# Optimization experiments

Measured on AMD Instinct MI355X. Metric: run time of the kernel, lower is better.

## Reference

```python
import jax, jax.numpy as jnp
import numpy as np

INPUT_DIM, HIDDEN_DIM, N_CLASSES = 512, 256, 2
TOP_RATIO, MIN_PATCHES, K_INST = 0.7, 128, 8
B, N = 4, 16384


def setup_inputs() -> dict:
    key = jax.random.key(0)
    ks = jax.random.split(key, 10)
    D, H, C = INPUT_DIM, HIDDEN_DIM, N_CLASSES
    s = lambda fan: 1.0 / np.sqrt(fan)
    return {
        "features": jax.random.normal(ks[0], (B, N, D), dtype=jnp.float32),
        # attention_net: Linear(D->H) (dropout is identity in eval)
        "Wa": jax.random.uniform(ks[1], (D, H), minval=-s(D), maxval=s(D), dtype=jnp.float32),
        "ba": jax.random.uniform(ks[2], (H,), minval=-s(D), maxval=s(D), dtype=jnp.float32),
        # per-class attention branches: Linear(H->1), stacked over classes
        "Wbr": jax.random.uniform(ks[3], (C, H), minval=-s(H), maxval=s(H), dtype=jnp.float32),
        "bbr": jax.random.uniform(ks[4], (C,), minval=-s(H), maxval=s(H), dtype=jnp.float32),
        # per-class instance classifiers: Linear(D->H) -> ReLU -> Linear(H->2)
        "W1": jax.random.uniform(ks[5], (C, D, H), minval=-s(D), maxval=s(D), dtype=jnp.float32),
        "b1": jax.random.uniform(ks[6], (C, H), minval=-s(D), maxval=s(D), dtype=jnp.float32),
        "W2": jax.random.uniform(ks[7], (C, H, 2), minval=-s(H), maxval=s(H), dtype=jnp.float32),
        "b2": jax.random.uniform(ks[8], (C, 2), minval=-s(H), maxval=s(H), dtype=jnp.float32),
    }


def reference(features, Wa, ba, Wbr, bbr, W1, b1, W2, b2):
    Bb, Nn, D = features.shape
    C = Wbr.shape[0]

    # ---- compute_attention ----
    h = jax.nn.relu(features @ Wa + ba)                       # (B,N,H)
    a_logits = jnp.einsum('bnh,ch->bcn', h, Wbr) + bbr[None, :, None]
    attn_all = jax.nn.softmax(a_logits, axis=-1)              # (B,C,N)
    combined = attn_all.mean(axis=1)                          # (B,N)

    # ---- per-sample top-k selection (k static under jit) ----
    k = min(max(int(Nn * TOP_RATIO), MIN_PATCHES), Nn)
    _, sel_idx = jax.lax.top_k(combined, k)                   # (B,k)
    sel_idx = jnp.sort(sel_idx, axis=-1)
    selected = jnp.take_along_axis(features, sel_idx[..., None], axis=1)  # (B,k,D)

    # ---- instance clustering loss (vectorized over B x C) ----
    kk = min(K_INST, Nn // 2)
    _, top_idx = jax.lax.top_k(attn_all, kk)                  # (B,C,kk)
    _, bot_idx = jax.lax.top_k(-attn_all, kk)                 # largest=False
    both_idx = jnp.concatenate([top_idx, bot_idx], axis=-1)   # (B,C,2kk)
    inst = features[jnp.arange(Bb)[:, None, None], both_idx]  # (B,C,2kk,D)
    h1 = jax.nn.relu(jnp.einsum('bckd,cdh->bckh', inst, W1) + b1[None, :, None, :])
    logits = jnp.einsum('bckh,cho->bcko', h1, W2) + b2[None, :, None, :]  # (B,C,2kk,2)
    labels = jnp.concatenate([jnp.ones(kk, jnp.int32), jnp.zeros(kk, jnp.int32)])
    logp = jax.nn.log_softmax(logits, axis=-1)
    ce = -jnp.take_along_axis(
        logp, jnp.broadcast_to(labels[None, None, :, None], (Bb, C, 2 * kk, 1)), axis=-1
    )[..., 0]                                                 # (B,C,2kk)
    cl_loss = ce.mean(axis=-1).sum() / (Bb * C)

    return selected, combined, sel_idx, cl_loss
```

## Files before the change

### kernel.cpp

```cpp
#include <hip/hip_runtime.h>

#define NB 4
#define NP 16384
#define DD 512
#define HH 256
#define CC 2
#define KSEL 11468
#define TOTP (NB*NP)
#define BCAP 4096

#define OFF_COMB (NB*KSEL*DD)
#define OFF_IDX  (OFF_COMB + NB*NP)
#define OFF_LOSS (OFF_IDX + NB*KSEL)

#define WS_ALOGIT 0
#define WS_ATTN   (NB*CC*NP)
#define WS_SELIDX (2*NB*CC*NP)
#define WS_MZ     (WS_SELIDX + NB*KSEL)
#define WS_BCNT   (WS_MZ + 16)
#define WS_BLIST  (WS_BCNT + 4)
#define WS_TOP16  (WS_BLIST + NB*BCAP)
#define WS_CE     (WS_TOP16 + 128)

typedef __attribute__((ext_vector_type(8))) short short8x;
typedef __attribute__((ext_vector_type(4))) float f32x4;

__device__ __forceinline__ unsigned short f2bf(float x){
  unsigned u = __float_as_uint(x);
  unsigned r = (u + 0x7FFFu + ((u >> 16) & 1u)) >> 16;
  return (unsigned short)r;
}

__global__ __launch_bounds__(256) void waconv_kernel(
    const float* __restrict__ Wa, unsigned short* __restrict__ WaT)
{
  __shared__ float tile[32][33];
  const int tx = threadIdx.x, ty = threadIdx.y;
  const int k0 = blockIdx.x * 32, n0 = blockIdx.y * 32;
  #pragma unroll
  for (int i=0;i<4;++i)
    tile[ty+8*i][tx] = Wa[(size_t)(k0+ty+8*i)*HH + n0 + tx];
  __syncthreads();
  #pragma unroll
  for (int i=0;i<4;++i)
    WaT[(size_t)(n0+ty+8*i)*DD + k0 + tx] = f2bf(tile[tx][ty+8*i]);
}

__global__ __launch_bounds__(512) void gemm_mfma_kernel(
    const float* __restrict__ feat, const unsigned short* __restrict__ WaT,
    const float* __restrict__ ba, const float* __restrict__ Wbr,
    const float* __restrict__ bbr, float* __restrict__ aL)
{
  __shared__ __attribute__((aligned(16))) unsigned char smem[65536];
  __shared__ float sBA[HH], sW0[HH], sW1[HH];
  unsigned char* sA = smem;
  unsigned char* sB = smem + 16384;

  const int tid  = threadIdx.x;
  const int lane = tid & 63;
  const int wid  = tid >> 6;
  const int wm = wid >> 2, wn = wid & 3;
  const int fr = lane & 15, fq = lane >> 4;
  const int p0 = blockIdx.x * 128;
  const float bb0 = bbr[0], bb1 = bbr[1];

  if (tid < HH){ sBA[tid] = ba[tid]; sW0[tid] = Wbr[tid]; sW1[tid] = Wbr[HH+tid]; }

  f32x4 acc[4][4];
  #pragma unroll
  for (int i=0;i<4;++i)
    #pragma unroll
    for (int j=0;j<4;++j)
      acc[i][j] = (f32x4){0.f,0.f,0.f,0.f};

  const int am = tid >> 2, akq = (tid & 3) * 16;
  const int bn = tid >> 1, bhf = tid & 1;

  for (int k0 = 0; k0 < DD; k0 += 64){
    __syncthreads();
    {
      const float4* src = reinterpret_cast<const float4*>(
          feat + (size_t)(p0 + am)*DD + k0 + akq);
      float4 v0 = src[0], v1 = src[1], v2 = src[2], v3 = src[3];
      unsigned short u[16];
      u[0]=f2bf(v0.x); u[1]=f2bf(v0.y); u[2]=f2bf(v0.z); u[3]=f2bf(v0.w);
      u[4]=f2bf(v1.x); u[5]=f2bf(v1.y); u[6]=f2bf(v1.z); u[7]=f2bf(v1.w);
      u[8]=f2bf(v2.x); u[9]=f2bf(v2.y); u[10]=f2bf(v2.z); u[11]=f2bf(v2.w);
      u[12]=f2bf(v3.x); u[13]=f2bf(v3.y); u[14]=f2bf(v3.z); u[15]=f2bf(v3.w);
      uint4 w0, w1;
      w0.x = (unsigned)u[0] | ((unsigned)u[1]<<16);
      w0.y = (unsigned)u[2] | ((unsigned)u[3]<<16);
      w0.z = (unsigned)u[4] | ((unsigned)u[5]<<16);
      w0.w = (unsigned)u[6] | ((unsigned)u[7]<<16);
      w1.x = (unsigned)u[8] | ((unsigned)u[9]<<16);
      w1.y = (unsigned)u[10] | ((unsigned)u[11]<<16);
      w1.z = (unsigned)u[12] | ((unsigned)u[13]<<16);
      w1.w = (unsigned)u[14] | ((unsigned)u[15]<<16);
      const int swz = (am & 7) << 4;
      *reinterpret_cast<uint4*>(sA + (((am*128) + akq*2) ^ swz)) = w0;
      *reinterpret_cast<uint4*>(sA + (((am*128) + akq*2 + 16) ^ swz)) = w1;
    }
    {
      const uint4* src = reinterpret_cast<const uint4*>(
          WaT + (size_t)bn*DD + k0 + bhf*32);
      uint4 q0 = src[0], q1 = src[1], q2 = src[2], q3 = src[3];
      const int swz = (bn & 7) << 4;
      const int base = bn*128 + bhf*64;
      *reinterpret_cast<uint4*>(sB + ((base     ) ^ swz)) = q0;
      *reinterpret_cast<uint4*>(sB + ((base + 16) ^ swz)) = q1;
      *reinterpret_cast<uint4*>(sB + ((base + 32) ^ swz)) = q2;
      *reinterpret_cast<uint4*>(sB + ((base + 48) ^ swz)) = q3;
    }
    __syncthreads();
    #pragma unroll
    for (int kf = 0; kf < 2; ++kf){
      short8x af[4], bf[4];
      #pragma unroll
      for (int mf = 0; mf < 4; ++mf){
        int m_loc = wm*64 + mf*16 + fr;
        int off = ((m_loc*128 + kf*64 + fq*16) ^ ((m_loc & 7) << 4));
        af[mf] = *reinterpret_cast<const short8x*>(sA + off);
      }
      #pragma unroll
      for (int nf = 0; nf < 4; ++nf){
        int n_loc = wn*64 + nf*16 + fr;
        int off = ((n_loc*128 + kf*64 + fq*16) ^ ((n_loc & 7) << 4));
        bf[nf] = *reinterpret_cast<const short8x*>(sB + off);
      }
      #pragma unroll
      for (int mf = 0; mf < 4; ++mf)
        #pragma unroll
        for (int nf = 0; nf < 4; ++nf)
          acc[mf][nf] = __builtin_amdgcn_mfma_f32_16x16x32_bf16(
              af[mf], bf[nf], acc[mf][nf], 0, 0, 0);
    }
  }
  __syncthreads();

  float* hS = reinterpret_cast<float*>(smem);
  #pragma unroll
  for (int mh = 0; mh < 2; ++mh){
    if (wm == mh){
      #pragma unroll
      for (int mf = 0; mf < 4; ++mf)
        #pragma unroll
        for (int nf = 0; nf < 4; ++nf)
          #pragma unroll
          for (int r = 0; r < 4; ++r){
            int row = mf*16 + fq*4 + r;
            int col = wn*64 + nf*16 + fr;
            hS[row*256 + col] = acc[mf][nf][r];
          }
    }
    __syncthreads();
    {
      const int row = tid >> 3, cg = tid & 7;
      float s0 = 0.f, s1 = 0.f;
      #pragma unroll
      for (int j = 0; j < 8; ++j){
        int col = cg*4 + j*32;
        float4 hv = *reinterpret_cast<const float4*>(&hS[row*256 + col]);
        float xs[4] = {hv.x, hv.y, hv.z, hv.w};
        #pragma unroll
        for (int u = 0; u < 4; ++u){
          int ccol = col + u;
          float x = fmaxf(xs[u] + sBA[ccol], 0.f);
          s0 += x * sW0[ccol];
          s1 += x * sW1[ccol];
        }
      }
      s0 += __shfl_xor(s0,1); s1 += __shfl_xor(s1,1);
      s0 += __shfl_xor(s0,2); s1 += __shfl_xor(s1,2);
      s0 += __shfl_xor(s0,4); s1 += __shfl_xor(s1,4);
      if (cg == 0){
        int p = p0 + mh*64 + row;
        int b = p >> 14, nl = p & (NP-1);
        aL[((size_t)b*CC + 0)*NP + nl] = s0 + bb0;
        aL[((size_t)b*CC + 1)*NP + nl] = s1 + bb1;
      }
    }
    __syncthreads();
  }
}

__global__ __launch_bounds__(1024) void smstat_kernel(
    const float* __restrict__ aL, float* __restrict__ mz)
{
  __shared__ float  s_redf[16];
  __shared__ double s_redd[16];
  __shared__ float  s_max;
  const int tid = threadIdx.x;
  const int lane = tid & 63, wid = tid >> 6;
  const int r = blockIdx.x;
  const float* a = aL + (size_t)r*NP;
  float m = -1e30f;
  for (int n=tid; n<NP; n+=1024) m = fmaxf(m, a[n]);
  #pragma unroll
  for (int off=1; off<64; off<<=1) m = fmaxf(m, __shfl_xor(m, off));
  if (lane==0) s_redf[wid]=m;
  __syncthreads();
  if (tid==0){ float mm=s_redf[0]; for(int w=1;w<16;++w) mm=fmaxf(mm,s_redf[w]); s_max=mm; }
  __syncthreads();
  m = s_max;
  double ls = 0.0;
  for (int n=tid;n<NP;n+=1024) ls += (double)expf(a[n]-m);
  #pragma unroll
  for (int off=1; off<64; off<<=1) ls += __shfl_xor(ls, off);
  if (lane==0) s_redd[wid]=ls;
  __syncthreads();
  if (tid==0){
    double t=0; for(int w=0;w<16;++w) t+=s_redd[w];
    mz[r*2+0]=m; mz[r*2+1]=(float)(1.0/t);
  }
}

__global__ __launch_bounds__(1024) void selTF_kernel(
    const float* __restrict__ aL, const float* __restrict__ mz,
    float* __restrict__ attn, float* __restrict__ comb,
    int* __restrict__ bcnt, int* __restrict__ blist)
{
  __shared__ unsigned s_red[2][16];
  __shared__ int s_cnt;
  const int tid = threadIdx.x;
  const int b = blockIdx.x;
  const int lane = tid & 63, wid = tid >> 6;
  const float m0 = mz[b*4+0], iz0 = mz[b*4+1], m1 = mz[b*4+2], iz1 = mz[b*4+3];
  const float* a0 = aL + ((size_t)b*CC + 0)*NP;
  const float* a1 = aL + ((size_t)b*CC + 1)*NP;
  float* o0 = attn + ((size_t)b*CC + 0)*NP;
  float* o1 = attn + ((size_t)b*CC + 1)*NP;
  float* oc = comb + (size_t)b*NP;
  const int n0 = tid*16;

  unsigned v[16];
  #pragma unroll
  for (int g=0; g<4; ++g){
    float4 qa = *reinterpret_cast<const float4*>(a0 + n0 + g*4);
    float4 qb = *reinterpret_cast<const float4*>(a1 + n0 + g*4);
    float4 E0, E1, CV;
    E0.x = expf(qa.x-m0)*iz0; E1.x = expf(qb.x-m1)*iz1; CV.x = 0.5f*(E0.x+E1.x);
    E0.y = expf(qa.y-m0)*iz0; E1.y = expf(qb.y-m1)*iz1; CV.y = 0.5f*(E0.y+E1.y);
    E0.z = expf(qa.z-m0)*iz0; E1.z = expf(qb.z-m1)*iz1; CV.z = 0.5f*(E0.z+E1.z);
    E0.w = expf(qa.w-m0)*iz0; E1.w = expf(qb.w-m1)*iz1; CV.w = 0.5f*(E0.w+E1.w);
    *reinterpret_cast<float4*>(o0 + n0 + g*4) = E0;
    *reinterpret_cast<float4*>(o1 + n0 + g*4) = E1;
    *reinterpret_cast<float4*>(oc + n0 + g*4) = CV;
    v[g*4+0]=__float_as_uint(CV.x);
    v[g*4+1]=__float_as_uint(CV.y);
    v[g*4+2]=__float_as_uint(CV.z);
    v[g*4+3]=__float_as_uint(CV.w);
  }
  if (tid==0) s_cnt = 0;

  unsigned cur = 0;
  #pragma unroll 1
  for (int bit=31; bit>=12; --bit){
    unsigned trial = cur | (1u<<bit);
    int c = 0;
    #pragma unroll
    for (int i=0;i<16;++i) c += (v[i] >= trial) ? 1 : 0;
    #pragma unroll
    for (int off=1; off<64; off<<=1) c += __shfl_xor(c, off);
    if (lane==0) s_red[bit&1][wid] = (unsigned)c;
    __syncthreads();
    unsigned tot=0;
    #pragma unroll
    for (int w=0;w<16;++w) tot += s_red[bit&1][w];
    if (tot >= KSEL) cur = trial;
  }
  const float Tv = __uint_as_float(cur);
  const float lo = Tv*0.989f, hi = Tv*1.0115f;
  #pragma unroll
  for (int i=0;i<16;++i){
    float x = __uint_as_float(v[i]);
    if (x >= lo && x <= hi){
      int s = atomicAdd(&s_cnt, 1);
      if (s < BCAP) blist[b*BCAP + s] = n0 + i;
    }
  }
  __syncthreads();
  if (tid==0) bcnt[b] = (s_cnt < BCAP) ? s_cnt : BCAP;
}

__global__ __launch_bounds__(256) void recomp_kernel(
    const float* __restrict__ feat, const float* __restrict__ Wa,
    const float* __restrict__ ba, const float* __restrict__ Wbr,
    const float* __restrict__ bbr, const float* __restrict__ mz,
    const int* __restrict__ bcnt, const int* __restrict__ blist,
    float* __restrict__ comb)
{
  __shared__ float fS[DD];
  __shared__ float r0[4], r1[4];
  const int tid = threadIdx.x;
  const int b = blockIdx.x >> 12;
  const int s = blockIdx.x & (BCAP-1);
  if (s >= bcnt[b]) return;
  const int lane = tid & 63, wid = tid >> 6;
  const float m0 = mz[b*4+0], iz0 = mz[b*4+1], m1 = mz[b*4+2], iz1 = mz[b*4+3];
  const int n = blist[b*BCAP + s];
  if (tid < 128){
    float4 v = *reinterpret_cast<const float4*>(feat + ((size_t)b*NP + n)*DD + tid*4);
    *reinterpret_cast<float4*>(&fS[tid*4]) = v;
  }
  __syncthreads();
  float a0=0.f,a1=0.f,a2=0.f,a3=0.f;
  #pragma unroll 4
  for (int d=0; d<DD; d+=4){
    a0 += fS[d+0]*Wa[(size_t)(d+0)*HH + tid];
    a1 += fS[d+1]*Wa[(size_t)(d+1)*HH + tid];
    a2 += fS[d+2]*Wa[(size_t)(d+2)*HH + tid];
    a3 += fS[d+3]*Wa[(size_t)(d+3)*HH + tid];
  }
  float h = fmaxf((a0+a1)+(a2+a3) + ba[tid], 0.f);
  float p0 = h*Wbr[tid], p1 = h*Wbr[HH+tid];
  #pragma unroll
  for (int off=1; off<64; off<<=1){ p0+=__shfl_xor(p0,off); p1+=__shfl_xor(p1,off); }
  if (lane==0){ r0[wid]=p0; r1[wid]=p1; }
  __syncthreads();
  if (tid==0){
    float l0 = (r0[0]+r0[1])+(r0[2]+r0[3]) + bbr[0];
    float l1 = (r1[0]+r1[1])+(r1[2]+r1[3]) + bbr[1];
    comb[(size_t)b*NP + n] = 0.5f*(expf(l0-m0)*iz0 + expf(l1-m1)*iz1);
  }
}

__global__ __launch_bounds__(1024) void select_kernel(
    const float* __restrict__ comb, float* __restrict__ outIdxF,
    int* __restrict__ selIdx)
{
  __shared__ unsigned s_red[2][16];
  __shared__ unsigned s_wsum[16];
  const int tid = threadIdx.x;
  const int b = blockIdx.x;
  const int lane = tid & 63, wid = tid >> 6;
  const float* row = comb + (size_t)b*NP;

  unsigned v[16];
  {
    const float4* rp = reinterpret_cast<const float4*>(row + tid*16);
    #pragma unroll
    for (int g=0; g<4; ++g){
      float4 q = rp[g];
      v[g*4+0]=__float_as_uint(q.x);
      v[g*4+1]=__float_as_uint(q.y);
      v[g*4+2]=__float_as_uint(q.z);
      v[g*4+3]=__float_as_uint(q.w);
    }
  }
  unsigned cur = 0;
  #pragma unroll 1
  for (int bit=31; bit>=0; --bit){
    unsigned trial = cur | (1u<<bit);
    int c = 0;
    #pragma unroll
    for (int i=0;i<16;++i) c += (v[i] >= trial) ? 1 : 0;
    #pragma unroll
    for (int off=1; off<64; off<<=1) c += __shfl_xor(c, off);
    if (lane==0) s_red[bit&1][wid] = (unsigned)c;
    __syncthreads();
    unsigned tot=0;
    #pragma unroll
    for (int w=0;w<16;++w) tot += s_red[bit&1][w];
    if (tot >= KSEL) cur = trial;
  }
  const unsigned T = cur;
  {
    int c = 0;
    #pragma unroll
    for (int i=0;i<16;++i) c += (v[i] > T) ? 1 : 0;
    #pragma unroll
    for (int off=1; off<64; off<<=1) c += __shfl_xor(c, off);
    if (lane==0) s_red[1][wid] = (unsigned)c;
  }
  __syncthreads();
  unsigned gtot=0;
  #pragma unroll
  for (int w=0;w<16;++w) gtot += s_red[1][w];
  const int extra = KSEL - (int)gtot;

  int eqc=0;
  #pragma unroll
  for (int i=0;i<16;++i) eqc += (v[i]==T) ? 1 : 0;
  unsigned inc = (unsigned)eqc;
  #pragma unroll
  for (int off=1; off<64; off<<=1){
    unsigned o = __shfl_up(inc, off);
    if (lane >= off) inc += o;
  }
  if (lane==63) s_wsum[wid] = inc;
  __syncthreads();
  unsigned wbase = 0;
  for (int w=0; w<wid; ++w) wbase += s_wsum[w];
  const int eqBase = (int)(wbase + inc) - eqc;

  int eq=eqBase, sc=0;
  #pragma unroll
  for (int i=0;i<16;++i){
    unsigned x = v[i];
    if (x==T){ if (eq<extra) sc++; eq++; }
    else if (x>T) sc++;
  }
  unsigned inc2 = (unsigned)sc;
  #pragma unroll
  for (int off=1; off<64; off<<=1){
    unsigned o = __shfl_up(inc2, off);
    if (lane >= off) inc2 += o;
  }
  __syncthreads();
  if (lane==63) s_wsum[wid] = inc2;
  __syncthreads();
  unsigned wbase2 = 0;
  for (int w=0; w<wid; ++w) wbase2 += s_wsum[w];
  int pos = (int)(wbase2 + inc2) - sc;

  eq=eqBase;
  #pragma unroll
  for (int i=0;i<16;++i){
    unsigned x = v[i];
    int f=0;
    if (x==T){ if (eq<extra) f=1; eq++; }
    else if (x>T) f=1;
    if (f){
      int n = tid*16 + i;
      outIdxF[(size_t)b*KSEL + pos] = (float)n;
      selIdx[(size_t)b*KSEL + pos] = n;
      pos++;
    }
  }
}

__global__ __launch_bounds__(256) void gather_kernel(
    const float* __restrict__ feat, const int* __restrict__ selIdx,
    float* __restrict__ outSel)
{
  const int tid = threadIdx.x;
  const int row = blockIdx.x*2 + (tid>>7);
  const int c4 = tid & 127;
  const int b = row / KSEL;
  const int idx = selIdx[row];
  const float4 v = *reinterpret_cast<const float4*>(feat + ((size_t)b*NP + idx)*DD + c4*4);
  *reinterpret_cast<float4*>(outSel + (size_t)row*DD + c4*4) = v;
}

__global__ __launch_bounds__(256) void top16_kernel(
    const float* __restrict__ attn, int* __restrict__ top16)
{
  __shared__ unsigned long long wkT[4][8];
  __shared__ unsigned long long wkB[4][8];
  const int tid = threadIdx.x;
  const int bid = blockIdx.x;
  const int lane = tid & 63, wid = tid >> 6;
  const float* a = attn + (size_t)bid*NP;

  unsigned long long t8[8], b8[8];
  #pragma unroll
  for (int i=0;i<8;++i){ t8[i]=0ull; b8[i]=~0ull; }

  for (int j=0;j<16;++j){
    const int n4 = tid + 256*j;
    const float4 v = *reinterpret_cast<const float4*>(a + 4*n4);
    const float xs[4] = {v.x, v.y, v.z, v.w};
    #pragma unroll
    for (int q=0;q<4;++q){
      const int n = 4*n4 + q;
      const unsigned vb = __float_as_uint(xs[q]);
      unsigned long long kt = ((unsigned long long)vb<<32) | (unsigned)(NP-1-n);
      if (kt > t8[7]){
        t8[7]=kt;
        #pragma unroll
        for (int i=7;i>0;--i){ if (t8[i]>t8[i-1]){ unsigned long long t=t8[i-1]; t8[i-1]=t8[i]; t8[i]=t; } }
      }
      unsigned long long kb = ((unsigned long long)vb<<32) | (unsigned)n;
      if (kb < b8[7]){
        b8[7]=kb;
        #pragma unroll
        for (int i=7;i>0;--i){ if (b8[i]<b8[i-1]){ unsigned long long t=b8[i-1]; b8[i-1]=b8[i]; b8[i]=t; } }
      }
    }
  }

  #pragma unroll
  for (int pick=0; pick<8; ++pick){
    unsigned long long loc = t8[0];
    #pragma unroll
    for (int i=1;i<8;++i) loc = t8[i]>loc ? t8[i] : loc;
    #pragma unroll
    for (int off=1; off<64; off<<=1){ unsigned long long o=__shfl_xor(loc,off); loc=o>loc?o:loc; }
    if (lane==0) wkT[wid][pick]=loc;
    #pragma unroll
    for (int i=0;i<8;++i) if (t8[i]==loc) t8[i]=0ull;
  }
  #pragma unroll
  for (int pick=0; pick<8; ++pick){
    unsigned long long loc = b8[0];
    #pragma unroll
    for (int i=1;i<8;++i) loc = b8[i]<loc ? b8[i] : loc;
    #pragma unroll
    for (int off=1; off<64; off<<=1){ unsigned long long o=__shfl_xor(loc,off); loc=o<loc?o:loc; }
    if (lane==0) wkB[wid][pick]=loc;
    #pragma unroll
    for (int i=0;i<8;++i) if (b8[i]==loc) b8[i]=~0ull;
  }
  __syncthreads();

  if (wid==0){
    unsigned long long k = (lane<32) ? wkT[lane>>3][lane&7] : 0ull;
    #pragma unroll
    for (int pick=0; pick<8; ++pick){
      unsigned long long loc = k;
      #pragma unroll
      for (int off=1; off<64; off<<=1){ unsigned long long o=__shfl_xor(loc,off); loc=o>loc?o:loc; }
      if (k==loc) k=0ull;
      if (lane==0) top16[bid*16+pick] = NP-1-(int)(loc & 0xFFFFFFFFull);
    }
    unsigned long long kb = (lane<32) ? wkB[lane>>3][lane&7] : ~0ull;
    #pragma unroll
    for (int pick=0; pick<8; ++pick){
      unsigned long long loc = kb;
      #pragma unroll
      for (int off=1; off<64; off<<=1){ unsigned long long o=__shfl_xor(loc,off); loc=o<loc?o:loc; }
      if (kb==loc) kb=~0ull;
      if (lane==0) top16[bid*16+8+pick] = (int)(loc & 0xFFFFFFFFull);
    }
  }
}

__global__ __launch_bounds__(256) void mlp_kernel(
    const float* __restrict__ feat, const float* __restrict__ W1,
    const float* __restrict__ b1, const float* __restrict__ W2,
    const float* __restrict__ b2, const int* __restrict__ top16,
    float* __restrict__ cews)
{
  __shared__ float fS[DD];
  __shared__ float r0[4], r1[4];
  const int tid = threadIdx.x;
  const int bid = blockIdx.x;
  const int r = bid & 15, c = (bid >> 4) & 1, b = bid >> 5;
  const int lane = tid & 63, wid = tid >> 6;
  const int gi = top16[(b*2+c)*16 + r];
  if (tid < 128){
    float4 v = *reinterpret_cast<const float4*>(feat + ((size_t)b*NP + gi)*DD + tid*4);
    *reinterpret_cast<float4*>(&fS[tid*4]) = v;
  }
  __syncthreads();
  const float* w1c = W1 + (size_t)c*DD*HH;
  float a0=0.f,a1=0.f,a2=0.f,a3=0.f;
  #pragma unroll 4
  for (int d=0; d<DD; d+=4){
    a0 += fS[d+0]*w1c[(size_t)(d+0)*HH + tid];
    a1 += fS[d+1]*w1c[(size_t)(d+1)*HH + tid];
    a2 += fS[d+2]*w1c[(size_t)(d+2)*HH + tid];
    a3 += fS[d+3]*w1c[(size_t)(d+3)*HH + tid];
  }
  float h = fmaxf((a0+a1)+(a2+a3) + b1[c*HH+tid], 0.f);
  float p0 = h*W2[(size_t)(c*HH+tid)*2 + 0];
  float p1 = h*W2[(size_t)(c*HH+tid)*2 + 1];
  #pragma unroll
  for (int off=1; off<64; off<<=1){ p0+=__shfl_xor(p0,off); p1+=__shfl_xor(p1,off); }
  if (lane==0){ r0[wid]=p0; r1[wid]=p1; }
  __syncthreads();
  if (tid==0){
    float l0 = (r0[0]+r0[1])+(r0[2]+r0[3]) + b2[c*2+0];
    float l1 = (r1[0]+r1[1])+(r1[2]+r1[3]) + b2[c*2+1];
    float mm = fmaxf(l0,l1);
    float lse = mm + logf(expf(l0-mm)+expf(l1-mm));
    float chosen = (r<8) ? l1 : l0;
    cews[bid] = lse - chosen;
  }
}

__global__ void loss_kernel(const float* __restrict__ cews, float* __restrict__ out_loss){
  if (threadIdx.x==0 && blockIdx.x==0){
    float s=0.f;
    for (int i=0;i<128;++i) s += cews[i];
    out_loss[0] = s / 128.0f;
  }
}

extern "C" void kernel_launch(void* const* d_in, const int* in_sizes, int n_in,
                              void* d_out, int out_size, void* d_ws, size_t ws_size,
                              hipStream_t stream) {
  const float* feat = (const float*)d_in[0];
  const float* Wa   = (const float*)d_in[1];
  const float* ba   = (const float*)d_in[2];
  const float* Wbr  = (const float*)d_in[3];
  const float* bbr  = (const float*)d_in[4];
  const float* W1   = (const float*)d_in[5];
  const float* b1   = (const float*)d_in[6];
  const float* W2   = (const float*)d_in[7];
  const float* b2   = (const float*)d_in[8];
  float* out = (float*)d_out;
  float* ws  = (float*)d_ws;

  float* a_logits = ws + WS_ALOGIT;
  float* attn     = ws + WS_ATTN;
  int*   selIdx   = (int*)(ws + WS_SELIDX);
  float* mz       = ws + WS_MZ;
  int*   bcnt     = (int*)(ws + WS_BCNT);
  int*   blist    = (int*)(ws + WS_BLIST);
  int*   top16    = (int*)(ws + WS_TOP16);
  float* cews     = ws + WS_CE;

  unsigned short* WaT = (unsigned short*)d_out;

  hipLaunchKernelGGL(waconv_kernel, dim3(DD/32, HH/32), dim3(32,8), 0, stream,
                     Wa, WaT);
  hipLaunchKernelGGL(gemm_mfma_kernel, dim3(TOTP/128), dim3(512), 0, stream,
                     feat, WaT, ba, Wbr, bbr, a_logits);
  hipLaunchKernelGGL(smstat_kernel, dim3(NB*CC), dim3(1024), 0, stream,
                     a_logits, mz);
  hipLaunchKernelGGL(selTF_kernel, dim3(NB), dim3(1024), 0, stream,
                     a_logits, mz, attn, out + OFF_COMB, bcnt, blist);
  hipLaunchKernelGGL(recomp_kernel, dim3(NB*BCAP), dim3(256), 0, stream,
                     feat, Wa, ba, Wbr, bbr, mz, bcnt, blist, out + OFF_COMB);
  hipLaunchKernelGGL(select_kernel, dim3(NB), dim3(1024), 0, stream,
                     out + OFF_COMB, out + OFF_IDX, selIdx);
  hipLaunchKernelGGL(gather_kernel, dim3(NB*KSEL/2), dim3(256), 0, stream,
                     feat, selIdx, out);
  hipLaunchKernelGGL(top16_kernel, dim3(NB*CC), dim3(256), 0, stream,
                     attn, top16);
  hipLaunchKernelGGL(mlp_kernel, dim3(NB*CC*16), dim3(256), 0, stream,
                     feat, W1, b1, W2, b2, top16, cews);
  hipLaunchKernelGGL(loss_kernel, dim3(1), dim3(64), 0, stream,
                     cews, out + OFF_LOSS);
}
```

Baseline: 275.3 us.

## Batch boundary recompute 16 rows per block and drop attn materialization

The boundary recompute kernel now handles 16 candidate rows per 512-thread block instead of one row per block. Each 32-lane group computes one row with float4 loads of Wa and 8 accumulators, so every Wa read is shared across far more work and launch overhead drops. The attn buffer is no longer written by selTF; top16 recomputes the softmax from logits and the softmax stats instead. This saves 512KB of writes in exchange for extra expf work in a small kernel.

```diff
diff --git a/kernel.cpp b/kernel.cpp
--- a/kernel.cpp
+++ b/kernel.cpp
@@ -14,7 +14,6 @@
 #define OFF_LOSS (OFF_IDX + NB*KSEL)
 
 #define WS_ALOGIT 0
-#define WS_ATTN   (NB*CC*NP)
 #define WS_SELIDX (2*NB*CC*NP)
 #define WS_MZ     (WS_SELIDX + NB*KSEL)
 #define WS_BCNT   (WS_MZ + 16)
@@ -216,8 +215,7 @@
 
 __global__ __launch_bounds__(1024) void selTF_kernel(
     const float* __restrict__ aL, const float* __restrict__ mz,
-    float* __restrict__ attn, float* __restrict__ comb,
-    int* __restrict__ bcnt, int* __restrict__ blist)
+    float* __restrict__ comb, int* __restrict__ bcnt, int* __restrict__ blist)
 {
   __shared__ unsigned s_red[2][16];
   __shared__ int s_cnt;
@@ -227,8 +225,6 @@
   const float m0 = mz[b*4+0], iz0 = mz[b*4+1], m1 = mz[b*4+2], iz1 = mz[b*4+3];
   const float* a0 = aL + ((size_t)b*CC + 0)*NP;
   const float* a1 = aL + ((size_t)b*CC + 1)*NP;
-  float* o0 = attn + ((size_t)b*CC + 0)*NP;
-  float* o1 = attn + ((size_t)b*CC + 1)*NP;
   float* oc = comb + (size_t)b*NP;
   const int n0 = tid*16;
 
@@ -237,13 +233,11 @@
   for (int g=0; g<4; ++g){
     float4 qa = *reinterpret_cast<const float4*>(a0 + n0 + g*4);
     float4 qb = *reinterpret_cast<const float4*>(a1 + n0 + g*4);
-    float4 E0, E1, CV;
-    E0.x = expf(qa.x-m0)*iz0; E1.x = expf(qb.x-m1)*iz1; CV.x = 0.5f*(E0.x+E1.x);
-    E0.y = expf(qa.y-m0)*iz0; E1.y = expf(qb.y-m1)*iz1; CV.y = 0.5f*(E0.y+E1.y);
-    E0.z = expf(qa.z-m0)*iz0; E1.z = expf(qb.z-m1)*iz1; CV.z = 0.5f*(E0.z+E1.z);
-    E0.w = expf(qa.w-m0)*iz0; E1.w = expf(qb.w-m1)*iz1; CV.w = 0.5f*(E0.w+E1.w);
-    *reinterpret_cast<float4*>(o0 + n0 + g*4) = E0;
-    *reinterpret_cast<float4*>(o1 + n0 + g*4) = E1;
+    float4 CV;
+    CV.x = 0.5f*(expf(qa.x-m0)*iz0 + expf(qb.x-m1)*iz1);
+    CV.y = 0.5f*(expf(qa.y-m0)*iz0 + expf(qb.y-m1)*iz1);
+    CV.z = 0.5f*(expf(qa.z-m0)*iz0 + expf(qb.z-m1)*iz1);
+    CV.w = 0.5f*(expf(qa.w-m0)*iz0 + expf(qb.w-m1)*iz1);
     *reinterpret_cast<float4*>(oc + n0 + g*4) = CV;
     v[g*4+0]=__float_as_uint(CV.x);
     v[g*4+1]=__float_as_uint(CV.y);
@@ -282,45 +276,71 @@
   if (tid==0) bcnt[b] = (s_cnt < BCAP) ? s_cnt : BCAP;
 }
 
-__global__ __launch_bounds__(256) void recomp_kernel(
+__global__ __launch_bounds__(512) void recomp_kernel(
     const float* __restrict__ feat, const float* __restrict__ Wa,
     const float* __restrict__ ba, const float* __restrict__ Wbr,
     const float* __restrict__ bbr, const float* __restrict__ mz,
     const int* __restrict__ bcnt, const int* __restrict__ blist,
     float* __restrict__ comb)
 {
-  __shared__ float fS[DD];
-  __shared__ float r0[4], r1[4];
+  __shared__ float fS[16][DD];
+  __shared__ int   s_n[16];
   const int tid = threadIdx.x;
-  const int b = blockIdx.x >> 12;
-  const int s = blockIdx.x & (BCAP-1);
-  if (s >= bcnt[b]) return;
-  const int lane = tid & 63, wid = tid >> 6;
-  const float m0 = mz[b*4+0], iz0 = mz[b*4+1], m1 = mz[b*4+2], iz1 = mz[b*4+3];
-  const int n = blist[b*BCAP + s];
-  if (tid < 128){
-    float4 v = *reinterpret_cast<const float4*>(feat + ((size_t)b*NP + n)*DD + tid*4);
-    *reinterpret_cast<float4*>(&fS[tid*4]) = v;
-  }
-  __syncthreads();
-  float a0=0.f,a1=0.f,a2=0.f,a3=0.f;
-  #pragma unroll 4
+  const int b  = blockIdx.x >> 8;
+  const int g0 = (blockIdx.x & 255) * 16;
+  const int cnt = bcnt[b];
+  if (g0 >= cnt) return;
+  if (tid < 16)
+    s_n[tid] = (g0 + tid < cnt) ? blist[b*BCAP + g0 + tid] : -1;
+  __syncthreads();
+  #pragma unroll
+  for (int pass=0; pass<4; ++pass){
+    const int j = pass*4 + (tid>>7);
+    const int c4 = (tid & 127)*4;
+    const int n = s_n[j];
+    if (n >= 0){
+      float4 v = *reinterpret_cast<const float4*>(feat + ((size_t)b*NP + n)*DD + c4);
+      *reinterpret_cast<float4*>(&fS[j][c4]) = v;
+    }
+  }
+  __syncthreads();
+
+  const int grp = tid >> 5, l32 = tid & 31;
+  if (s_n[grp] < 0) return;
+  const int h0 = l32*4;
+  float acc[8];
+  #pragma unroll
+  for (int i=0;i<8;++i) acc[i]=0.f;
+
   for (int d=0; d<DD; d+=4){
-    a0 += fS[d+0]*Wa[(size_t)(d+0)*HH + tid];
-    a1 += fS[d+1]*Wa[(size_t)(d+1)*HH + tid];
-    a2 += fS[d+2]*Wa[(size_t)(d+2)*HH + tid];
-    a3 += fS[d+3]*Wa[(size_t)(d+3)*HH + tid];
-  }
-  float h = fmaxf((a0+a1)+(a2+a3) + ba[tid], 0.f);
-  float p0 = h*Wbr[tid], p1 = h*Wbr[HH+tid];
-  #pragma unroll
-  for (int off=1; off<64; off<<=1){ p0+=__shfl_xor(p0,off); p1+=__shfl_xor(p1,off); }
-  if (lane==0){ r0[wid]=p0; r1[wid]=p1; }
-  __syncthreads();
-  if (tid==0){
-    float l0 = (r0[0]+r0[1])+(r0[2]+r0[3]) + bbr[0];
-    float l1 = (r1[0]+r1[1])+(r1[2]+r1[3]) + bbr[1];
-    comb[(size_t)b*NP + n] = 0.5f*(expf(l0-m0)*iz0 + expf(l1-m1)*iz1);
+    const float4 f4 = *reinterpret_cast<const float4*>(&fS[grp][d]);
+    const float fx[4] = {f4.x, f4.y, f4.z, f4.w};
+    #pragma unroll
+    for (int u=0; u<4; ++u){
+      const float* wr = Wa + (size_t)(d+u)*HH;
+      float4 wa0 = *reinterpret_cast<const float4*>(wr + h0);
+      float4 wa1 = *reinterpret_cast<const float4*>(wr + 128 + h0);
+      acc[0] += fx[u]*wa0.x; acc[1] += fx[u]*wa0.y;
+      acc[2] += fx[u]*wa0.z; acc[3] += fx[u]*wa0.w;
+      acc[4] += fx[u]*wa1.x; acc[5] += fx[u]*wa1.y;
+      acc[6] += fx[u]*wa1.z; acc[7] += fx[u]*wa1.w;
+    }
+  }
+  float p0 = 0.f, p1 = 0.f;
+  #pragma unroll
+  for (int i=0;i<8;++i){
+    const int h = (i<4) ? (h0+i) : (128 + h0 + (i-4));
+    float x = fmaxf(acc[i] + ba[h], 0.f);
+    p0 += x * Wbr[h];
+    p1 += x * Wbr[HH+h];
+  }
+  #pragma unroll
+  for (int off=1; off<32; off<<=1){ p0+=__shfl_xor(p0,off); p1+=__shfl_xor(p1,off); }
+  if (l32==0){
+    const float m0 = mz[b*4+0], iz0 = mz[b*4+1], m1 = mz[b*4+2], iz1 = mz[b*4+3];
+    float l0 = p0 + bbr[0];
+    float l1 = p1 + bbr[1];
+    comb[(size_t)b*NP + s_n[grp]] = 0.5f*(expf(l0-m0)*iz0 + expf(l1-m1)*iz1);
   }
 }
 
@@ -443,14 +463,16 @@
 }
 
 __global__ __launch_bounds__(256) void top16_kernel(
-    const float* __restrict__ attn, int* __restrict__ top16)
+    const float* __restrict__ aL, const float* __restrict__ mz,
+    int* __restrict__ top16)
 {
   __shared__ unsigned long long wkT[4][8];
   __shared__ unsigned long long wkB[4][8];
   const int tid = threadIdx.x;
   const int bid = blockIdx.x;
   const int lane = tid & 63, wid = tid >> 6;
-  const float* a = attn + (size_t)bid*NP;
+  const float* a = aL + (size_t)bid*NP;
+  const float m = mz[bid*2+0], iz = mz[bid*2+1];
 
   unsigned long long t8[8], b8[8];
   #pragma unroll
@@ -459,7 +481,9 @@
   for (int j=0;j<16;++j){
     const int n4 = tid + 256*j;
     const float4 v = *reinterpret_cast<const float4*>(a + 4*n4);
-    const float xs[4] = {v.x, v.y, v.z, v.w};
+    float xs[4];
+    xs[0] = expf(v.x-m)*iz; xs[1] = expf(v.y-m)*iz;
+    xs[2] = expf(v.z-m)*iz; xs[3] = expf(v.w-m)*iz;
     #pragma unroll
     for (int q=0;q<4;++q){
       const int n = 4*n4 + q;
@@ -593,7 +617,6 @@
   float* ws  = (float*)d_ws;
 
   float* a_logits = ws + WS_ALOGIT;
-  float* attn     = ws + WS_ATTN;
   int*   selIdx   = (int*)(ws + WS_SELIDX);
   float* mz       = ws + WS_MZ;
   int*   bcnt     = (int*)(ws + WS_BCNT);
@@ -610,15 +633,15 @@
   hipLaunchKernelGGL(smstat_kernel, dim3(NB*CC), dim3(1024), 0, stream,
                      a_logits, mz);
   hipLaunchKernelGGL(selTF_kernel, dim3(NB), dim3(1024), 0, stream,
-                     a_logits, mz, attn, out + OFF_COMB, bcnt, blist);
-  hipLaunchKernelGGL(recomp_kernel, dim3(NB*BCAP), dim3(256), 0, stream,
+                     a_logits, mz, out + OFF_COMB, bcnt, blist);
+  hipLaunchKernelGGL(recomp_kernel, dim3(NB*256), dim3(512), 0, stream,
                      feat, Wa, ba, Wbr, bbr, mz, bcnt, blist, out + OFF_COMB);
   hipLaunchKernelGGL(select_kernel, dim3(NB), dim3(1024), 0, stream,
                      out + OFF_COMB, out + OFF_IDX, selIdx);
   hipLaunchKernelGGL(gather_kernel, dim3(NB*KSEL/2), dim3(256), 0, stream,
                      feat, selIdx, out);
   hipLaunchKernelGGL(top16_kernel, dim3(NB*CC), dim3(256), 0, stream,
-                     attn, top16);
+                     a_logits, mz, top16);
   hipLaunchKernelGGL(mlp_kernel, dim3(NB*CC*16), dim3(256), 0, stream,
                      feat, W1, b1, W2, b2, top16, cews);
   hipLaunchKernelGGL(loss_kernel, dim3(1), dim3(64), 0, stream,
```

Result: slower. 380.3 us (+38.1%).
